# Kernel optimization log

Measured on AMD Instinct MI355X. Metric: run time of the kernel, lower is better.

## Reference

```python
import jax, jax.numpy as jnp
import numpy as np

N, E = 100000, 1600000
FEAT, HID, MSG, OUT, GOAL = 32, 64, 32, 8, 16
EPS = 1e-5


def _bn(x, gamma, beta):
    # BatchNorm1d in training mode: batch mean + biased variance
    mu = jnp.mean(x, axis=0)
    var = jnp.var(x, axis=0)
    return gamma * (x - mu) * jax.lax.rsqrt(var + EPS) + beta


def setup_inputs() -> dict:
    key = jax.random.key(0)
    ks = jax.random.split(key, 12)
    inp = {
        "nodes": jax.random.normal(ks[0], (N, FEAT), dtype=jnp.float32),
        "goal": jax.random.normal(ks[1], (N, GOAL), dtype=jnp.float32),
        "edge_src": jax.random.randint(ks[2], (E,), 0, N, dtype=jnp.int32),
        "edge_dst": jax.random.randint(ks[3], (E,), 0, N, dtype=jnp.int32),
        "send_input": 1,
        "get_output": 1,
        # InputModel: Linear(FEAT->HID) + ReLU + BN
        "W_in": jax.random.normal(ks[4], (FEAT, HID), dtype=jnp.float32) * 0.1,
        "b_in": jnp.zeros((HID,), dtype=jnp.float32),
        "g_in": jnp.ones((HID,), dtype=jnp.float32),
        "be_in": jnp.zeros((HID,), dtype=jnp.float32),
        # MessageModel: Linear(HID->MSG) + ReLU + BN
        "W_msg": jax.random.normal(ks[5], (HID, MSG), dtype=jnp.float32) * 0.1,
        "b_msg": jnp.zeros((MSG,), dtype=jnp.float32),
        "g_msg": jnp.ones((MSG,), dtype=jnp.float32),
        "be_msg": jnp.zeros((MSG,), dtype=jnp.float32),
        # UpdateModel (goal_opt=1): Linear(MSG+HID+GOAL->HID) + ReLU + BN
        "W_upd": jax.random.normal(ks[6], (MSG + HID + GOAL, HID), dtype=jnp.float32) * 0.1,
        "b_upd": jnp.zeros((HID,), dtype=jnp.float32),
        "g_upd": jnp.ones((HID,), dtype=jnp.float32),
        "be_upd": jnp.zeros((HID,), dtype=jnp.float32),
        # OutputModel (no goal): Linear(HID->OUT)
        "W_out": jax.random.normal(ks[7], (HID, OUT), dtype=jnp.float32) * 0.1,
        "b_out": jnp.zeros((OUT,), dtype=jnp.float32),
    }
    return inp


def reference(nodes, goal, edge_src, edge_dst, send_input, get_output,
              W_in, b_in, g_in, be_in,
              W_msg, b_msg, g_msg, be_msg,
              W_upd, b_upd, g_upd, be_upd,
              W_out, b_out):
    # InputModel
    if send_input:
        h = _bn(jax.nn.relu(nodes @ W_in + b_in), g_in, be_in)  # [N, HID]
    else:
        h = nodes
    # MessageModel
    m = _bn(jax.nn.relu(h @ W_msg + b_msg), g_msg, be_msg)      # [N, MSG]
    # _aggregate: gather predecessor messages, sum per destination node
    agg = jax.ops.segment_sum(m[edge_src], edge_dst, num_segments=N)  # [N, MSG]
    # UpdateModel (goal_opt=1 -> concat goal)
    cat = jnp.concatenate([agg, h, goal], axis=1)               # [N, MSG+HID+GOAL]
    u = _bn(jax.nn.relu(cat @ W_upd + b_upd), g_upd, be_upd)    # [N, HID]
    if get_output:
        out = u @ W_out + b_out                                  # [N, OUT]
        return (u, out)
    return (u, None)
```

## Files before the change

### kernel.cpp

```cpp
#include <hip/hip_runtime.h>
#include <stdint.h>

#define NN 100000
#define EE 1600000
#define FEAT 32
#define HID 64
#define MSG 32
#define GOALD 16
#define OUTD 8
#define UPD_IN 112
#define EPS 1e-5f

__global__ __launch_bounds__(256) void k_in_stats(
    const float* __restrict__ nodes, const float* __restrict__ W_in,
    const float* __restrict__ b_in, float* __restrict__ stats1)
{
    __shared__ float red[256];
    const int tid = threadIdx.x;
    const int j = tid & 63, slot = tid >> 6;
    float w[FEAT];
#pragma unroll
    for (int k = 0; k < FEAT; ++k) w[k] = W_in[k * HID + j];
    const float bj = b_in[j];
    float lsum = 0.f, lsq = 0.f;
    for (int i = blockIdx.x * 4 + slot; i < NN; i += gridDim.x * 4) {
        const float4* row = (const float4*)(nodes + (size_t)i * FEAT);
        float acc = bj;
#pragma unroll
        for (int q = 0; q < FEAT / 4; ++q) {
            float4 r = row[q];
            acc = fmaf(r.x, w[q * 4 + 0], acc);
            acc = fmaf(r.y, w[q * 4 + 1], acc);
            acc = fmaf(r.z, w[q * 4 + 2], acc);
            acc = fmaf(r.w, w[q * 4 + 3], acc);
        }
        float v = fmaxf(acc, 0.f);
        lsum += v; lsq += v * v;
    }
    red[tid] = lsum; __syncthreads();
    if (tid < 64) atomicAdd(&stats1[tid], red[tid] + red[tid + 64] + red[tid + 128] + red[tid + 192]);
    __syncthreads();
    red[tid] = lsq; __syncthreads();
    if (tid < 64) atomicAdd(&stats1[64 + tid], red[tid] + red[tid + 64] + red[tid + 128] + red[tid + 192]);
}

__global__ __launch_bounds__(256) void k_h_msg(
    const float* __restrict__ nodes, const float* __restrict__ W_in,
    const float* __restrict__ b_in, const float* __restrict__ stats1,
    const float* __restrict__ g_in, const float* __restrict__ be_in,
    const float* __restrict__ W_msg, const float* __restrict__ b_msg,
    float* __restrict__ h_out, float* __restrict__ x2_out,
    float* __restrict__ stats2)
{
    __shared__ float shh[4][HID];
    __shared__ float red[256];
    const int tid = threadIdx.x;
    const int j = tid & 63, slot = tid >> 6;
    const int j2 = j & 31, half = j >> 5;
    float w[FEAT];
#pragma unroll
    for (int k = 0; k < FEAT; ++k) w[k] = W_in[k * HID + j];
    float wm[32];
#pragma unroll
    for (int k = 0; k < 32; ++k) wm[k] = W_msg[(half * 32 + k) * MSG + j2];
    const float bj = b_in[j];
    const float m1 = stats1[j] * (1.f / NN);
    const float va1 = stats1[HID + j] * (1.f / NN) - m1 * m1;
    const float s1 = g_in[j] * rsqrtf(va1 + EPS);
    const float t1 = be_in[j] - m1 * s1;
    const float bm = b_msg[j2];
    float lsum = 0.f, lsq = 0.f;
    for (int base = blockIdx.x * 4; base < NN; base += gridDim.x * 4) {
        const int i = base + slot;
        const bool act = i < NN;
        float hv = 0.f;
        if (act) {
            const float4* row = (const float4*)(nodes + (size_t)i * FEAT);
            float acc = bj;
#pragma unroll
            for (int q = 0; q < FEAT / 4; ++q) {
                float4 r = row[q];
                acc = fmaf(r.x, w[q * 4 + 0], acc);
                acc = fmaf(r.y, w[q * 4 + 1], acc);
                acc = fmaf(r.z, w[q * 4 + 2], acc);
                acc = fmaf(r.w, w[q * 4 + 3], acc);
            }
            hv = fmaf(fmaxf(acc, 0.f), s1, t1);
            h_out[(size_t)i * HID + j] = hv;
        }
        shh[slot][j] = hv;
        __syncthreads();
        if (act) {
            const float4* hr = (const float4*)(&shh[slot][half * 32]);
            float acc2 = 0.f;
#pragma unroll
            for (int q = 0; q < 8; ++q) {
                float4 r = hr[q];
                acc2 = fmaf(r.x, wm[q * 4 + 0], acc2);
                acc2 = fmaf(r.y, wm[q * 4 + 1], acc2);
                acc2 = fmaf(r.z, wm[q * 4 + 2], acc2);
                acc2 = fmaf(r.w, wm[q * 4 + 3], acc2);
            }
            acc2 += __shfl_xor(acc2, 32);
            if (half == 0) {
                float v = fmaxf(acc2 + bm, 0.f);
                x2_out[(size_t)i * MSG + j2] = v;
                lsum += v; lsq += v * v;
            }
        }
        __syncthreads();
    }
    red[tid] = (half == 0) ? lsum : 0.f; __syncthreads();
    if (tid < 32) atomicAdd(&stats2[tid], red[tid] + red[tid + 64] + red[tid + 128] + red[tid + 192]);
    __syncthreads();
    red[tid] = (half == 0) ? lsq : 0.f; __syncthreads();
    if (tid < 32) atomicAdd(&stats2[32 + tid], red[tid] + red[tid + 64] + red[tid + 128] + red[tid + 192]);
}

__global__ __launch_bounds__(256) void k_build(
    const int* __restrict__ esrc, const int* __restrict__ edst,
    int* __restrict__ head, int2* __restrict__ pair)
{
    const int stride = gridDim.x * blockDim.x;
    for (int e = blockIdx.x * blockDim.x + threadIdx.x; e < EE; e += stride) {
        const int s = esrc[e], d = edst[e];
        const int old = atomicExch(&head[d], e);
        pair[e] = make_int2(s, old);
    }
}

__global__ __launch_bounds__(256) void k_agg_chain(
    const int* __restrict__ head, const int2* __restrict__ pair,
    const float* __restrict__ x2, const float* __restrict__ stats2,
    const float* __restrict__ g_msg, const float* __restrict__ be_msg,
    float* __restrict__ aggout)
{
    const int c = threadIdx.x & 31;
    const int hw = (blockIdx.x * blockDim.x + threadIdx.x) >> 5;
    const int nhw = (gridDim.x * blockDim.x) >> 5;
    const float m = stats2[c] * (1.f / NN);
    const float va = stats2[MSG + c] * (1.f / NN) - m * m;
    const float s = g_msg[c] * rsqrtf(va + EPS);
    const float t = be_msg[c] - m * s;
    for (int i0 = hw; i0 < NN; i0 += 2 * nhw) {
        const int i1 = i0 + nhw;
        int e0 = head[i0];
        int e1 = (i1 < NN) ? head[i1] : -1;
        float S0 = 0.f, S1 = 0.f;
        int d0 = 0, d1 = 0;
        while (e0 >= 0 || e1 >= 0) {
            if (e0 >= 0) {
                const int2 p0 = pair[e0];
                S0 += x2[(size_t)p0.x * MSG + c];
                e0 = p0.y; ++d0;
            }
            if (e1 >= 0) {
                const int2 p1 = pair[e1];
                S1 += x2[(size_t)p1.x * MSG + c];
                e1 = p1.y; ++d1;
            }
        }
        aggout[(size_t)i0 * HID + c] = fmaf(s, S0, (float)d0 * t);
        if (i1 < NN)
            aggout[(size_t)i1 * HID + c] = fmaf(s, S1, (float)d1 * t);
    }
}

__global__ __launch_bounds__(256) void k_upd(
    float* __restrict__ aggx3, const float* __restrict__ h,
    const float* __restrict__ goal, const float* __restrict__ W_upd,
    const float* __restrict__ b_upd, float* __restrict__ stats3)
{
    __shared__ float cat[4][UPD_IN];
    __shared__ float red[256];
    const int tid = threadIdx.x;
    const int j = tid & 63, slot = tid >> 6;
    float w[UPD_IN];
#pragma unroll
    for (int k = 0; k < UPD_IN; ++k) w[k] = W_upd[k * HID + j];
    const float bj = b_upd[j];
    float lsum = 0.f, lsq = 0.f;
    for (int base = blockIdx.x * 4; base < NN; base += gridDim.x * 4) {
        const int i = base + slot;
        const bool act = i < NN;
        if (act) {
            if (j < 32) cat[slot][j] = aggx3[(size_t)i * HID + j];
            cat[slot][32 + j] = h[(size_t)i * HID + j];
            if (j < 16) cat[slot][96 + j] = goal[(size_t)i * GOALD + j];
        }
        __syncthreads();
        if (act) {
            const float4* cr = (const float4*)cat[slot];
            float acc = bj;
#pragma unroll
            for (int q = 0; q < UPD_IN / 4; ++q) {
                float4 r = cr[q];
                acc = fmaf(r.x, w[q * 4 + 0], acc);
                acc = fmaf(r.y, w[q * 4 + 1], acc);
                acc = fmaf(r.z, w[q * 4 + 2], acc);
                acc = fmaf(r.w, w[q * 4 + 3], acc);
            }
            float v = fmaxf(acc, 0.f);
            aggx3[(size_t)i * HID + j] = v;
            lsum += v; lsq += v * v;
        }
        __syncthreads();
    }
    red[tid] = lsum; __syncthreads();
    if (tid < 64) atomicAdd(&stats3[tid], red[tid] + red[tid + 64] + red[tid + 128] + red[tid + 192]);
    __syncthreads();
    red[tid] = lsq; __syncthreads();
    if (tid < 64) atomicAdd(&stats3[64 + tid], red[tid] + red[tid + 64] + red[tid + 128] + red[tid + 192]);
}

__global__ __launch_bounds__(256) void k_out(
    float* __restrict__ x3u, const float* __restrict__ stats3,
    const float* __restrict__ g_upd, const float* __restrict__ be_upd,
    const float* __restrict__ W_out, const float* __restrict__ b_out,
    float* __restrict__ o_out)
{
    __shared__ float shu[4][HID];
    const int tid = threadIdx.x;
    const int j = tid & 63, slot = tid >> 6;
    const int o = j & 7, part = j >> 3;
    const float m3 = stats3[j] * (1.f / NN);
    const float va3 = stats3[HID + j] * (1.f / NN) - m3 * m3;
    const float s3 = g_upd[j] * rsqrtf(va3 + EPS);
    const float t3 = be_upd[j] - m3 * s3;
    float w[8];
#pragma unroll
    for (int k = 0; k < 8; ++k) w[k] = W_out[(part * 8 + k) * OUTD + o];
    const float bo = b_out[o];
    for (int base = blockIdx.x * 4; base < NN; base += gridDim.x * 4) {
        const int i = base + slot;
        const bool act = i < NN;
        float u = 0.f;
        if (act) {
            u = fmaf(x3u[(size_t)i * HID + j], s3, t3);
            x3u[(size_t)i * HID + j] = u;
        }
        shu[slot][j] = u;
        __syncthreads();
        if (act) {
            const float* ur = &shu[slot][part * 8];
            float acc = 0.f;
#pragma unroll
            for (int k = 0; k < 8; ++k) acc = fmaf(ur[k], w[k], acc);
            acc += __shfl_xor(acc, 8);
            acc += __shfl_xor(acc, 16);
            acc += __shfl_xor(acc, 32);
            if (part == 0) o_out[(size_t)i * OUTD + o] = acc + bo;
        }
        __syncthreads();
    }
}

extern "C" void kernel_launch(void* const* d_in, const int* in_sizes, int n_in,
                              void* d_out, int out_size, void* d_ws, size_t ws_size,
                              hipStream_t stream)
{
    (void)in_sizes; (void)n_in; (void)out_size;
    const float* nodes  = (const float*)d_in[0];
    const float* goal   = (const float*)d_in[1];
    const int*   esrc   = (const int*)d_in[2];
    const int*   edst   = (const int*)d_in[3];
    const float* W_in   = (const float*)d_in[6];
    const float* b_in   = (const float*)d_in[7];
    const float* g_in   = (const float*)d_in[8];
    const float* be_in  = (const float*)d_in[9];
    const float* W_msg  = (const float*)d_in[10];
    const float* b_msg  = (const float*)d_in[11];
    const float* g_msg  = (const float*)d_in[12];
    const float* be_msg = (const float*)d_in[13];
    const float* W_upd  = (const float*)d_in[14];
    const float* b_upd  = (const float*)d_in[15];
    const float* g_upd  = (const float*)d_in[16];
    const float* be_upd = (const float*)d_in[17];
    const float* W_out  = (const float*)d_in[18];
    const float* b_out  = (const float*)d_in[19];

    const size_t need = (320 + (size_t)NN * 96) * sizeof(float)
                      + (size_t)NN * sizeof(int) + (size_t)EE * sizeof(int2);
    if (ws_size < need) return;

    float* st = (float*)d_ws;
    float* stats1 = st;
    float* stats2 = st + 128;
    float* stats3 = st + 192;
    float* h  = st + 320;
    float* x2 = h + (size_t)NN * 64;
    int*  head = (int*)(x2 + (size_t)NN * 32);
    int2* pair = (int2*)(head + NN);

    float* u_out = (float*)d_out;
    float* o_out = (float*)d_out + (size_t)NN * HID;

    hipMemsetAsync(st, 0, 320 * sizeof(float), stream);
    hipMemsetAsync(head, 0xFF, NN * sizeof(int), stream);

    k_build<<<2048, 256, 0, stream>>>(esrc, edst, head, pair);
    k_in_stats<<<1024, 256, 0, stream>>>(nodes, W_in, b_in, stats1);
    k_h_msg<<<1024, 256, 0, stream>>>(nodes, W_in, b_in, stats1, g_in, be_in,
                                      W_msg, b_msg, h, x2, stats2);
    k_agg_chain<<<2048, 256, 0, stream>>>(head, pair, x2, stats2, g_msg, be_msg, u_out);
    k_upd<<<1024, 256, 0, stream>>>(u_out, h, goal, W_upd, b_upd, stats3);
    k_out<<<1024, 256, 0, stream>>>(u_out, stats3, g_upd, be_upd, W_out, b_out, o_out);
}
```

Measured before the change: 480.7 us.

## Store messages as packed bf16 for gather and merge build with input stats

The message activations x2 are now stored as packed bf16 pairs, so each gathered row in the edge aggregation is half the bytes. Each lane of a 16-lane group handles two channels and accumulates in fp32. The edge linked-list build and the input-layer statistics kernel are merged into one launch with disjoint block ranges, removing a launch and letting the two overlap. The cost is bf16 rounding of the messages before summation, which may affect accuracy tolerance.

```diff
diff --git a/kernel.cpp b/kernel.cpp
--- a/kernel.cpp
+++ b/kernel.cpp
@@ -11,37 +11,54 @@
 #define UPD_IN 112
 #define EPS 1e-5f
 
-__global__ __launch_bounds__(256) void k_in_stats(
+__device__ inline unsigned bf16rne(float f) {
+    unsigned u = __float_as_uint(f);
+    return (u + 0x7FFF + ((u >> 16) & 1)) >> 16;
+}
+
+__global__ __launch_bounds__(256) void k_pre(
+    const int* __restrict__ esrc, const int* __restrict__ edst,
+    int* __restrict__ head, int2* __restrict__ pair,
     const float* __restrict__ nodes, const float* __restrict__ W_in,
     const float* __restrict__ b_in, float* __restrict__ stats1)
 {
-    __shared__ float red[256];
-    const int tid = threadIdx.x;
-    const int j = tid & 63, slot = tid >> 6;
-    float w[FEAT];
-#pragma unroll
-    for (int k = 0; k < FEAT; ++k) w[k] = W_in[k * HID + j];
-    const float bj = b_in[j];
-    float lsum = 0.f, lsq = 0.f;
-    for (int i = blockIdx.x * 4 + slot; i < NN; i += gridDim.x * 4) {
-        const float4* row = (const float4*)(nodes + (size_t)i * FEAT);
-        float acc = bj;
-#pragma unroll
-        for (int q = 0; q < FEAT / 4; ++q) {
-            float4 r = row[q];
-            acc = fmaf(r.x, w[q * 4 + 0], acc);
-            acc = fmaf(r.y, w[q * 4 + 1], acc);
-            acc = fmaf(r.z, w[q * 4 + 2], acc);
-            acc = fmaf(r.w, w[q * 4 + 3], acc);
-        }
-        float v = fmaxf(acc, 0.f);
-        lsum += v; lsq += v * v;
-    }
-    red[tid] = lsum; __syncthreads();
-    if (tid < 64) atomicAdd(&stats1[tid], red[tid] + red[tid + 64] + red[tid + 128] + red[tid + 192]);
-    __syncthreads();
-    red[tid] = lsq; __syncthreads();
-    if (tid < 64) atomicAdd(&stats1[64 + tid], red[tid] + red[tid + 64] + red[tid + 128] + red[tid + 192]);
+    if (blockIdx.x < 2048) {
+        const int stride = 2048 * 256;
+        for (int e = blockIdx.x * 256 + threadIdx.x; e < EE; e += stride) {
+            const int s = esrc[e], d = edst[e];
+            const int old = atomicExch(&head[d], e);
+            pair[e] = make_int2(s, old);
+        }
+    } else {
+        __shared__ float red[256];
+        const int bid = blockIdx.x - 2048;
+        const int tid = threadIdx.x;
+        const int j = tid & 63, slot = tid >> 6;
+        float w[FEAT];
+#pragma unroll
+        for (int k = 0; k < FEAT; ++k) w[k] = W_in[k * HID + j];
+        const float bj = b_in[j];
+        float lsum = 0.f, lsq = 0.f;
+        for (int i = bid * 4 + slot; i < NN; i += 1024 * 4) {
+            const float4* row = (const float4*)(nodes + (size_t)i * FEAT);
+            float acc = bj;
+#pragma unroll
+            for (int q = 0; q < FEAT / 4; ++q) {
+                float4 r = row[q];
+                acc = fmaf(r.x, w[q * 4 + 0], acc);
+                acc = fmaf(r.y, w[q * 4 + 1], acc);
+                acc = fmaf(r.z, w[q * 4 + 2], acc);
+                acc = fmaf(r.w, w[q * 4 + 3], acc);
+            }
+            float v = fmaxf(acc, 0.f);
+            lsum += v; lsq += v * v;
+        }
+        red[tid] = lsum; __syncthreads();
+        if (tid < 64) atomicAdd(&stats1[tid], red[tid] + red[tid + 64] + red[tid + 128] + red[tid + 192]);
+        __syncthreads();
+        red[tid] = lsq; __syncthreads();
+        if (tid < 64) atomicAdd(&stats1[64 + tid], red[tid] + red[tid + 64] + red[tid + 128] + red[tid + 192]);
+    }
 }
 
 __global__ __launch_bounds__(256) void k_h_msg(
@@ -49,7 +66,7 @@
     const float* __restrict__ b_in, const float* __restrict__ stats1,
     const float* __restrict__ g_in, const float* __restrict__ be_in,
     const float* __restrict__ W_msg, const float* __restrict__ b_msg,
-    float* __restrict__ h_out, float* __restrict__ x2_out,
+    float* __restrict__ h_out, unsigned* __restrict__ x2b_out,
     float* __restrict__ stats2)
 {
     __shared__ float shh[4][HID];
@@ -90,6 +107,7 @@
         }
         shh[slot][j] = hv;
         __syncthreads();
+        float v = 0.f;
         if (act) {
             const float4* hr = (const float4*)(&shh[slot][half * 32]);
             float acc2 = 0.f;
@@ -102,11 +120,13 @@
                 acc2 = fmaf(r.w, wm[q * 4 + 3], acc2);
             }
             acc2 += __shfl_xor(acc2, 32);
-            if (half == 0) {
-                float v = fmaxf(acc2 + bm, 0.f);
-                x2_out[(size_t)i * MSG + j2] = v;
-                lsum += v; lsq += v * v;
-            }
+            v = fmaxf(acc2 + bm, 0.f);
+            if (half == 0) { lsum += v; lsq += v * v; }
+        }
+        const float vn = __shfl_xor(v, 1);
+        if (act && half == 0 && (j2 & 1) == 0) {
+            const unsigned pk = bf16rne(v) | (bf16rne(vn) << 16);
+            x2b_out[(size_t)i * (MSG / 2) + (j2 >> 1)] = pk;
         }
         __syncthreads();
     }
@@ -117,52 +137,55 @@
     if (tid < 32) atomicAdd(&stats2[32 + tid], red[tid] + red[tid + 64] + red[tid + 128] + red[tid + 192]);
 }
 
-__global__ __launch_bounds__(256) void k_build(
-    const int* __restrict__ esrc, const int* __restrict__ edst,
-    int* __restrict__ head, int2* __restrict__ pair)
-{
-    const int stride = gridDim.x * blockDim.x;
-    for (int e = blockIdx.x * blockDim.x + threadIdx.x; e < EE; e += stride) {
-        const int s = esrc[e], d = edst[e];
-        const int old = atomicExch(&head[d], e);
-        pair[e] = make_int2(s, old);
-    }
-}
-
 __global__ __launch_bounds__(256) void k_agg_chain(
     const int* __restrict__ head, const int2* __restrict__ pair,
-    const float* __restrict__ x2, const float* __restrict__ stats2,
+    const unsigned* __restrict__ x2b, const float* __restrict__ stats2,
     const float* __restrict__ g_msg, const float* __restrict__ be_msg,
     float* __restrict__ aggout)
 {
-    const int c = threadIdx.x & 31;
-    const int hw = (blockIdx.x * blockDim.x + threadIdx.x) >> 5;
-    const int nhw = (gridDim.x * blockDim.x) >> 5;
-    const float m = stats2[c] * (1.f / NN);
-    const float va = stats2[MSG + c] * (1.f / NN) - m * m;
-    const float s = g_msg[c] * rsqrtf(va + EPS);
-    const float t = be_msg[c] - m * s;
-    for (int i0 = hw; i0 < NN; i0 += 2 * nhw) {
-        const int i1 = i0 + nhw;
+    const int l = threadIdx.x & 15;
+    const int c0 = l * 2, c1 = c0 + 1;
+    const int grp = (blockIdx.x * blockDim.x + threadIdx.x) >> 4;
+    const int ngrp = (gridDim.x * blockDim.x) >> 4;
+    const float m0 = stats2[c0] * (1.f / NN);
+    const float m1 = stats2[c1] * (1.f / NN);
+    const float va0 = stats2[MSG + c0] * (1.f / NN) - m0 * m0;
+    const float va1 = stats2[MSG + c1] * (1.f / NN) - m1 * m1;
+    const float s0 = g_msg[c0] * rsqrtf(va0 + EPS);
+    const float s1 = g_msg[c1] * rsqrtf(va1 + EPS);
+    const float t0 = be_msg[c0] - m0 * s0;
+    const float t1 = be_msg[c1] - m1 * s1;
+    for (int i0 = grp; i0 < NN; i0 += 2 * ngrp) {
+        const int i1 = i0 + ngrp;
         int e0 = head[i0];
         int e1 = (i1 < NN) ? head[i1] : -1;
-        float S0 = 0.f, S1 = 0.f;
+        float A0 = 0.f, B0 = 0.f, A1 = 0.f, B1 = 0.f;
         int d0 = 0, d1 = 0;
         while (e0 >= 0 || e1 >= 0) {
             if (e0 >= 0) {
-                const int2 p0 = pair[e0];
-                S0 += x2[(size_t)p0.x * MSG + c];
-                e0 = p0.y; ++d0;
+                const int2 p = pair[e0];
+                const unsigned pk = x2b[(size_t)p.x * (MSG / 2) + l];
+                A0 += __uint_as_float(pk << 16);
+                B0 += __uint_as_float(pk & 0xFFFF0000u);
+                e0 = p.y; ++d0;
             }
             if (e1 >= 0) {
-                const int2 p1 = pair[e1];
-                S1 += x2[(size_t)p1.x * MSG + c];
-                e1 = p1.y; ++d1;
-            }
-        }
-        aggout[(size_t)i0 * HID + c] = fmaf(s, S0, (float)d0 * t);
-        if (i1 < NN)
-            aggout[(size_t)i1 * HID + c] = fmaf(s, S1, (float)d1 * t);
+                const int2 p = pair[e1];
+                const unsigned pk = x2b[(size_t)p.x * (MSG / 2) + l];
+                A1 += __uint_as_float(pk << 16);
+                B1 += __uint_as_float(pk & 0xFFFF0000u);
+                e1 = p.y; ++d1;
+            }
+        }
+        float2 o;
+        o.x = fmaf(s0, A0, (float)d0 * t0);
+        o.y = fmaf(s1, B0, (float)d0 * t1);
+        ((float2*)(aggout + (size_t)i0 * HID))[l] = o;
+        if (i1 < NN) {
+            o.x = fmaf(s0, A1, (float)d1 * t0);
+            o.y = fmaf(s1, B1, (float)d1 * t1);
+            ((float2*)(aggout + (size_t)i1 * HID))[l] = o;
+        }
     }
 }
 
@@ -279,7 +302,7 @@
     const float* W_out  = (const float*)d_in[18];
     const float* b_out  = (const float*)d_in[19];
 
-    const size_t need = (320 + (size_t)NN * 96) * sizeof(float)
+    const size_t need = (320 + (size_t)NN * 80) * sizeof(float)
                       + (size_t)NN * sizeof(int) + (size_t)EE * sizeof(int2);
     if (ws_size < need) return;
 
@@ -288,8 +311,8 @@
     float* stats2 = st + 128;
     float* stats3 = st + 192;
     float* h  = st + 320;
-    float* x2 = h + (size_t)NN * 64;
-    int*  head = (int*)(x2 + (size_t)NN * 32);
+    unsigned* x2b = (unsigned*)(h + (size_t)NN * 64);
+    int*  head = (int*)(x2b + (size_t)NN * 16);
     int2* pair = (int2*)(head + NN);
 
     float* u_out = (float*)d_out;
@@ -298,11 +321,10 @@
     hipMemsetAsync(st, 0, 320 * sizeof(float), stream);
     hipMemsetAsync(head, 0xFF, NN * sizeof(int), stream);
 
-    k_build<<<2048, 256, 0, stream>>>(esrc, edst, head, pair);
-    k_in_stats<<<1024, 256, 0, stream>>>(nodes, W_in, b_in, stats1);
+    k_pre<<<3072, 256, 0, stream>>>(esrc, edst, head, pair, nodes, W_in, b_in, stats1);
     k_h_msg<<<1024, 256, 0, stream>>>(nodes, W_in, b_in, stats1, g_in, be_in,
-                                      W_msg, b_msg, h, x2, stats2);
-    k_agg_chain<<<2048, 256, 0, stream>>>(head, pair, x2, stats2, g_msg, be_msg, u_out);
+                                      W_msg, b_msg, h, x2b, stats2);
+    k_agg_chain<<<2048, 256, 0, stream>>>(head, pair, x2b, stats2, g_msg, be_msg, u_out);
     k_upd<<<1024, 256, 0, stream>>>(u_out, h, goal, W_upd, b_upd, stats3);
     k_out<<<1024, 256, 0, stream>>>(u_out, stats3, g_upd, be_upd, W_out, b_out, o_out);
 }
```

Result: faster. 445.2 us (-7.4%).
